# Optimization experiments

Measured on AMD Instinct MI355X. Metric: run time of the kernel, lower is better.

Reference implementation:

```python
import jax, jax.numpy as jnp
import numpy as np

N, E = 50000, 640000
DIN, DH, DOUT = 128, 256, 128


def _glorot(k, i, o):
    return jax.random.normal(k, (i, o), jnp.float32) / np.sqrt(i)


def setup_inputs() -> dict:
    key = jax.random.key(0)
    ks = jax.random.split(key, 12)
    return {
        "x": jax.random.normal(ks[0], (N, DIN), jnp.float32),
        "edge_index": jax.random.randint(ks[1], (2, E), 0, N, dtype=jnp.int32),
        # SAGEConv 1: in -> hidden (lin_l on aggregated w/ bias, lin_r on root)
        "W1l": _glorot(ks[2], DIN, DH), "b1l": jnp.zeros((DH,), jnp.float32), "W1r": _glorot(ks[3], DIN, DH),
        "g1": jnp.ones((DH,), jnp.float32), "be1": jnp.zeros((DH,), jnp.float32),
        # skip projection (in != hidden)
        "Wsk": _glorot(ks[4], DIN, DH), "bsk": jnp.zeros((DH,), jnp.float32),
        # SAGEConv 2: hidden -> hidden
        "W2l": _glorot(ks[5], DH, DH), "b2l": jnp.zeros((DH,), jnp.float32), "W2r": _glorot(ks[6], DH, DH),
        "g2": jnp.ones((DH,), jnp.float32), "be2": jnp.zeros((DH,), jnp.float32),
        # SAGEConv 3: hidden -> out
        "W3l": _glorot(ks[7], DH, DOUT), "b3l": jnp.zeros((DOUT,), jnp.float32), "W3r": _glorot(ks[8], DH, DOUT),
    }


def _sage_conv(x, src, dst, Wl, bl, Wr, n):
    # mean aggregation of source features into destination nodes
    msg = x[src]                                                 # [E, d]
    agg = jax.ops.segment_sum(msg, dst, num_segments=n)          # [N, d]
    cnt = jax.ops.segment_sum(jnp.ones((src.shape[0],), x.dtype), dst, num_segments=n)
    agg = agg / jnp.maximum(cnt, 1.0)[:, None]
    return agg @ Wl + bl + x @ Wr


def _layernorm(x, g, b):
    mu = jnp.mean(x, axis=-1, keepdims=True)
    var = jnp.mean((x - mu) ** 2, axis=-1, keepdims=True)
    return (x - mu) * jax.lax.rsqrt(var + 1e-5) * g + b


def reference(x, edge_index, W1l, b1l, W1r, g1, be1, Wsk, bsk,
              W2l, b2l, W2r, g2, be2, W3l, b3l, W3r):
    src, dst = edge_index[0], edge_index[1]
    n = x.shape[0]
    # layer 0: conv -> LN -> relu -> (dropout p=0, eval) -> skip via projection
    h = _sage_conv(x, src, dst, W1l, b1l, W1r, n)
    h = jax.nn.relu(_layernorm(h, g1, be1))
    h = h + (x @ Wsk + bsk)
    # layer 1: conv -> LN -> relu -> residual add (shapes match)
    h2 = _sage_conv(h, src, dst, W2l, b2l, W2r, n)
    h2 = jax.nn.relu(_layernorm(h2, g2, be2)) + h
    # final conv (no norm/act)
    return _sage_conv(h2, src, dst, W3l, b3l, W3r, n)
```

## Files before the change

### kernel.cpp

```cpp
#include <hip/hip_runtime.h>


typedef float floatx4 __attribute__((ext_vector_type(4)));
typedef short bf16x8 __attribute__((ext_vector_type(8)));

__device__ inline unsigned short f2bf(float f) {
    unsigned u = __float_as_uint(f);
    unsigned r = (u + 0x7fffu + ((u >> 16) & 1u)) >> 16;
    return (unsigned short)r;
}
__device__ inline float bf2f_lo(unsigned v) { return __uint_as_float(v << 16); }
__device__ inline float bf2f_hi(unsigned v) { return __uint_as_float(v & 0xffff0000u); }

__device__ inline void gl_lds16(const void* g, void* l) {
    __builtin_amdgcn_global_load_lds((const __attribute__((address_space(1))) unsigned int*)g,
                                     (__attribute__((address_space(3))) unsigned int*)l,
                                     16, 0, 0);
}

__global__ void hist_kernel(const int* __restrict__ dst, int* __restrict__ cnt, int E) {
    int i = blockIdx.x * blockDim.x + threadIdx.x;
    if (i < E) atomicAdd(&cnt[dst[i]], 1);
}

#define SCAN_CHUNK 2048

__global__ __launch_bounds__(256) void scan_blocksums(const int* __restrict__ cnt,
                                                      int* __restrict__ bsum, int N) {
    __shared__ int sh[256];
    int t = threadIdx.x;
    int base = blockIdx.x * SCAN_CHUNK + t * 8;
    int s = 0;
#pragma unroll
    for (int i = 0; i < 8; i++) {
        int idx = base + i;
        if (idx < N) s += cnt[idx];
    }
    sh[t] = s;
    __syncthreads();
    for (int off = 1; off < 256; off <<= 1) {
        int v = (t >= off) ? sh[t - off] : 0;
        __syncthreads();
        sh[t] += v;
        __syncthreads();
    }
    if (t == 255) bsum[blockIdx.x] = sh[255];
}

__global__ __launch_bounds__(256) void scan_bsums(const int* __restrict__ bsum,
                                                  int* __restrict__ boff, int NB,
                                                  int* __restrict__ rowptr, int N, int E) {
    __shared__ int sh[256];
    int t = threadIdx.x;
    int v = (t < NB) ? bsum[t] : 0;
    sh[t] = v;
    __syncthreads();
    for (int off = 1; off < 256; off <<= 1) {
        int u = (t >= off) ? sh[t - off] : 0;
        __syncthreads();
        sh[t] += u;
        __syncthreads();
    }
    if (t < NB) boff[t] = sh[t] - v;
    if (t == 0) rowptr[N] = E;
}

__global__ __launch_bounds__(256) void scan_final(const int* __restrict__ cnt,
                                                  const int* __restrict__ boff,
                                                  int* __restrict__ rowptr,
                                                  int* __restrict__ cursor,
                                                  float* __restrict__ invdeg, int N) {
    __shared__ int sh[256];
    int t = threadIdx.x;
    int base = blockIdx.x * SCAN_CHUNK + t * 8;
    int c[8];
    int s = 0;
#pragma unroll
    for (int i = 0; i < 8; i++) {
        int idx = base + i;
        c[i] = (idx < N) ? cnt[idx] : 0;
        s += c[i];
    }
    sh[t] = s;
    __syncthreads();
    for (int off = 1; off < 256; off <<= 1) {
        int v = (t >= off) ? sh[t - off] : 0;
        __syncthreads();
        sh[t] += v;
        __syncthreads();
    }
    int run = boff[blockIdx.x] + sh[t] - s;
#pragma unroll
    for (int i = 0; i < 8; i++) {
        int idx = base + i;
        if (idx < N) {
            rowptr[idx] = run;
            cursor[idx] = run;
            invdeg[idx] = 1.0f / (float)(c[i] > 1 ? c[i] : 1);
            run += c[i];
        }
    }
}

__global__ void scatter_kernel(const int* __restrict__ src, const int* __restrict__ dst,
                               int* __restrict__ cursor, int* __restrict__ col, int E) {
    int i = blockIdx.x * blockDim.x + threadIdx.x;
    if (i < E) {
        int p = atomicAdd(&cursor[dst[i]], 1);
        col[p] = src[i];
    }
}

__global__ void prep_weights(const float* __restrict__ W1l, const float* __restrict__ W1r,
                             const float* __restrict__ Wsk, const float* __restrict__ W2l,
                             const float* __restrict__ W2r, const float* __restrict__ W3l,
                             const float* __restrict__ W3r, const float* __restrict__ b1l,
                             const float* __restrict__ bsk,
                             unsigned short* __restrict__ WtC, unsigned short* __restrict__ Wt2,
                             unsigned short* __restrict__ Wt3, float* __restrict__ biasC) {
    int i = blockIdx.x * blockDim.x + threadIdx.x;
    if (i < 32768) {
        int k = i >> 8, n = i & 255;
        WtC[n * 256 + k] = f2bf(W1l[i]);
    } else if (i < 65536) {
        int j = i - 32768, k = j >> 8, n = j & 255;
        WtC[n * 256 + 128 + k] = f2bf(W1r[j]);
    } else if (i < 98304) {
        int j = i - 65536, k = j >> 8, n = j & 255;
        WtC[(256 + n) * 256 + 128 + k] = f2bf(Wsk[j]);
    } else if (i < 131072) {
        int j = i - 98304, k = j >> 8, n = j & 255;
        WtC[(256 + n) * 256 + k] = 0;
    } else if (i < 196608) {
        int j = i - 131072, k = j >> 8, n = j & 255;
        Wt2[n * 512 + k] = f2bf(W2l[j]);
    } else if (i < 262144) {
        int j = i - 196608, k = j >> 8, n = j & 255;
        Wt2[n * 512 + 256 + k] = f2bf(W2r[j]);
    } else if (i < 294912) {
        int j = i - 262144, k = j >> 7, n = j & 127;
        Wt3[n * 256 + k] = f2bf(W3l[j]);
    } else if (i < 327680) {
        int j = i - 294912, k = j >> 7, n = j & 127;
        Wt3[(128 + n) * 256 + k] = f2bf(W3r[j]);
    } else if (i < 328192) {
        int j = i - 327680;
        biasC[j] = (j < 256) ? b1l[j] : bsk[j - 256];
    }
}

__global__ void cvt_x_kernel(const float* __restrict__ x, unsigned short* __restrict__ A1cat, int total) {
    int i = blockIdx.x * blockDim.x + threadIdx.x;
    if (i >= total) return;
    int r = i >> 7, c = i & 127;
    A1cat[(size_t)r * 256 + 128 + c] = f2bf(x[i]);
}

__global__ __launch_bounds__(256) void agg_bf16_v2(const int* __restrict__ rowptr,
                                                   const int* __restrict__ col,
                                                   const float* __restrict__ invdeg,
                                                   const unsigned short* __restrict__ X, int xstride,
                                                   unsigned short* __restrict__ out, int ostride, int N) {
    int wid = (blockIdx.x * blockDim.x + threadIdx.x) >> 6;
    int lane = threadIdx.x & 63;
    if (wid >= N) return;
    int half = lane >> 5;
    int sub = lane & 31;
    int off = blockIdx.y * 128 + sub * 4;
    const unsigned short* Xo = X + off;
    int s = rowptr[wid], e = rowptr[wid + 1];
    float a0 = 0.f, a1 = 0.f, a2 = 0.f, a3 = 0.f;
    int j = s + half;
    for (; j + 6 < e; j += 8) {
        int c0 = col[j], c1 = col[j + 2], c2 = col[j + 4], c3 = col[j + 6];
        uint2 v0 = *(const uint2*)(Xo + (size_t)c0 * xstride);
        uint2 v1 = *(const uint2*)(Xo + (size_t)c1 * xstride);
        uint2 v2 = *(const uint2*)(Xo + (size_t)c2 * xstride);
        uint2 v3 = *(const uint2*)(Xo + (size_t)c3 * xstride);
        a0 += (bf2f_lo(v0.x) + bf2f_lo(v1.x)) + (bf2f_lo(v2.x) + bf2f_lo(v3.x));
        a1 += (bf2f_hi(v0.x) + bf2f_hi(v1.x)) + (bf2f_hi(v2.x) + bf2f_hi(v3.x));
        a2 += (bf2f_lo(v0.y) + bf2f_lo(v1.y)) + (bf2f_lo(v2.y) + bf2f_lo(v3.y));
        a3 += (bf2f_hi(v0.y) + bf2f_hi(v1.y)) + (bf2f_hi(v2.y) + bf2f_hi(v3.y));
    }
    for (; j < e; j += 2) {
        int c = col[j];
        uint2 v = *(const uint2*)(Xo + (size_t)c * xstride);
        a0 += bf2f_lo(v.x); a1 += bf2f_hi(v.x);
        a2 += bf2f_lo(v.y); a3 += bf2f_hi(v.y);
    }
    a0 += __shfl_xor(a0, 32, 64);
    a1 += __shfl_xor(a1, 32, 64);
    a2 += __shfl_xor(a2, 32, 64);
    a3 += __shfl_xor(a3, 32, 64);
    if (half == 0) {
        float inv = invdeg[wid];
        ushort4 o;
        o.x = f2bf(a0 * inv); o.y = f2bf(a1 * inv);
        o.z = f2bf(a2 * inv); o.w = f2bf(a3 * inv);
        *(ushort4*)(out + (size_t)wid * ostride + off) = o;
    }
}

__global__ __launch_bounds__(256) void agg_final_v2(const int* __restrict__ rowptr,
                                                    const int* __restrict__ col,
                                                    const float* __restrict__ invdeg,
                                                    const unsigned short* __restrict__ T,
                                                    const float* __restrict__ R,
                                                    float* __restrict__ out, int N) {
    int wid = (blockIdx.x * blockDim.x + threadIdx.x) >> 6;
    int lane = threadIdx.x & 63;
    if (wid >= N) return;
    int half = lane >> 5;
    int sub = lane & 31;
    const unsigned short* To = T + sub * 4;
    int s = rowptr[wid], e = rowptr[wid + 1];
    float a0 = 0.f, a1 = 0.f, a2 = 0.f, a3 = 0.f;
    int j = s + half;
    for (; j + 6 < e; j += 8) {
        int c0 = col[j], c1 = col[j + 2], c2 = col[j + 4], c3 = col[j + 6];
        uint2 v0 = *(const uint2*)(To + (size_t)c0 * 128);
        uint2 v1 = *(const uint2*)(To + (size_t)c1 * 128);
        uint2 v2 = *(const uint2*)(To + (size_t)c2 * 128);
        uint2 v3 = *(const uint2*)(To + (size_t)c3 * 128);
        a0 += (bf2f_lo(v0.x) + bf2f_lo(v1.x)) + (bf2f_lo(v2.x) + bf2f_lo(v3.x));
        a1 += (bf2f_hi(v0.x) + bf2f_hi(v1.x)) + (bf2f_hi(v2.x) + bf2f_hi(v3.x));
        a2 += (bf2f_lo(v0.y) + bf2f_lo(v1.y)) + (bf2f_lo(v2.y) + bf2f_lo(v3.y));
        a3 += (bf2f_hi(v0.y) + bf2f_hi(v1.y)) + (bf2f_hi(v2.y) + bf2f_hi(v3.y));
    }
    for (; j < e; j += 2) {
        int c = col[j];
        uint2 v = *(const uint2*)(To + (size_t)c * 128);
        a0 += bf2f_lo(v.x); a1 += bf2f_hi(v.x);
        a2 += bf2f_lo(v.y); a3 += bf2f_hi(v.y);
    }
    a0 += __shfl_xor(a0, 32, 64);
    a1 += __shfl_xor(a1, 32, 64);
    a2 += __shfl_xor(a2, 32, 64);
    a3 += __shfl_xor(a3, 32, 64);
    if (half == 0) {
        float inv = invdeg[wid];
        float4 r = *(const float4*)(R + (size_t)wid * 128 + sub * 4);
        float4 o;
        o.x = a0 * inv + r.x;
        o.y = a1 * inv + r.y;
        o.z = a2 * inv + r.z;
        o.w = a3 * inv + r.w;
        *(float4*)(out + (size_t)wid * 128 + sub * 4) = o;
    }
}

__device__ inline void store_out(float* p, float v) { *p = v; }
__device__ inline void store_out(unsigned short* p, float v) { *p = f2bf(v); }

template <typename OT>
__global__ __launch_bounds__(256) void gemm_mfma(const unsigned short* __restrict__ A, int lda, int K,
                                                 const unsigned short* __restrict__ B, int ldb,
                                                 const float* __restrict__ bias,
                                                 OT* __restrict__ C, int ldc, int M) {
    __shared__ unsigned short sA[128 * 64];
    __shared__ unsigned short sB[128 * 64];
    int t = threadIdx.x;
    int bm = blockIdx.x * 128;
    int bn = blockIdx.y * 128;
    int lane = t & 63;
    int w = t >> 6;
    int wm = (w >> 1) * 64, wn = (w & 1) * 64;

    floatx4 acc[4][4];
#pragma unroll
    for (int i = 0; i < 4; i++)
#pragma unroll
        for (int j = 0; j < 4; j++) acc[i][j] = (floatx4){0.f, 0.f, 0.f, 0.f};

    const int rA0 = t >> 3;
    const int kc8 = (t & 7) * 8;

    for (int k0 = 0; k0 < K; k0 += 64) {
#pragma unroll
        for (int i = 0; i < 4; i++) {
            int row = bm + rA0 + i * 32;
            if (row > M - 1) row = M - 1;
            gl_lds16(A + (size_t)row * lda + k0 + kc8, (void*)&sA[(size_t)(i * 256 + t) * 8]);
            gl_lds16(B + (size_t)(bn + rA0 + i * 32) * ldb + k0 + kc8,
                     (void*)&sB[(size_t)(i * 256 + t) * 8]);
        }
        __syncthreads();
#pragma unroll
        for (int ks = 0; ks < 2; ks++) {
            bf16x8 af[4], bfr[4];
#pragma unroll
            for (int mi = 0; mi < 4; mi++)
                af[mi] = *(const bf16x8*)&sA[(wm + mi * 16 + (lane & 15)) * 64 + ks * 32 + (lane >> 4) * 8];
#pragma unroll
            for (int ni = 0; ni < 4; ni++)
                bfr[ni] = *(const bf16x8*)&sB[(wn + ni * 16 + (lane & 15)) * 64 + ks * 32 + (lane >> 4) * 8];
#pragma unroll
            for (int mi = 0; mi < 4; mi++)
#pragma unroll
                for (int ni = 0; ni < 4; ni++)
                    acc[mi][ni] = __builtin_amdgcn_mfma_f32_16x16x32_bf16(af[mi], bfr[ni], acc[mi][ni], 0, 0, 0);
        }
        __syncthreads();
    }

    int col0 = bn + wn + (lane & 15);
    int rbase = bm + wm + (lane >> 4) * 4;
#pragma unroll
    for (int ni = 0; ni < 4; ni++) {
        int col = col0 + ni * 16;
        float bv = bias ? bias[col] : 0.f;
#pragma unroll
        for (int mi = 0; mi < 4; mi++) {
#pragma unroll
            for (int r = 0; r < 4; r++) {
                int row = rbase + mi * 16 + r;
                if (row < M) store_out(C + (size_t)row * ldc + col, acc[mi][ni][r] + bv);
            }
        }
    }
}

__global__ __launch_bounds__(256) void gemm_mfma_l3(const unsigned short* __restrict__ A, int lda, int K,
                                                    const unsigned short* __restrict__ B, int ldb,
                                                    const float* __restrict__ bias,
                                                    unsigned short* __restrict__ T,
                                                    float* __restrict__ R, int M) {
    __shared__ unsigned short sA[128 * 64];
    __shared__ unsigned short sB[128 * 64];
    int t = threadIdx.x;
    int bm = blockIdx.x * 128;
    int bn = blockIdx.y * 128;
    int lane = t & 63;
    int w = t >> 6;
    int wm = (w >> 1) * 64, wn = (w & 1) * 64;

    floatx4 acc[4][4];
#pragma unroll
    for (int i = 0; i < 4; i++)
#pragma unroll
        for (int j = 0; j < 4; j++) acc[i][j] = (floatx4){0.f, 0.f, 0.f, 0.f};

    const int rA0 = t >> 3;
    const int kc8 = (t & 7) * 8;

    for (int k0 = 0; k0 < K; k0 += 64) {
#pragma unroll
        for (int i = 0; i < 4; i++) {
            int row = bm + rA0 + i * 32;
            if (row > M - 1) row = M - 1;
            gl_lds16(A + (size_t)row * lda + k0 + kc8, (void*)&sA[(size_t)(i * 256 + t) * 8]);
            gl_lds16(B + (size_t)(bn + rA0 + i * 32) * ldb + k0 + kc8,
                     (void*)&sB[(size_t)(i * 256 + t) * 8]);
        }
        __syncthreads();
#pragma unroll
        for (int ks = 0; ks < 2; ks++) {
            bf16x8 af[4], bfr[4];
#pragma unroll
            for (int mi = 0; mi < 4; mi++)
                af[mi] = *(const bf16x8*)&sA[(wm + mi * 16 + (lane & 15)) * 64 + ks * 32 + (lane >> 4) * 8];
#pragma unroll
            for (int ni = 0; ni < 4; ni++)
                bfr[ni] = *(const bf16x8*)&sB[(wn + ni * 16 + (lane & 15)) * 64 + ks * 32 + (lane >> 4) * 8];
#pragma unroll
            for (int mi = 0; mi < 4; mi++)
#pragma unroll
                for (int ni = 0; ni < 4; ni++)
                    acc[mi][ni] = __builtin_amdgcn_mfma_f32_16x16x32_bf16(af[mi], bfr[ni], acc[mi][ni], 0, 0, 0);
        }
        __syncthreads();
    }

    int col0 = bn + wn + (lane & 15);
    int rbase = bm + wm + (lane >> 4) * 4;
#pragma unroll
    for (int ni = 0; ni < 4; ni++) {
        int col = col0 + ni * 16;
        if (col < 128) {
#pragma unroll
            for (int mi = 0; mi < 4; mi++)
#pragma unroll
                for (int r = 0; r < 4; r++) {
                    int row = rbase + mi * 16 + r;
                    if (row < M) T[(size_t)row * 128 + col] = f2bf(acc[mi][ni][r]);
                }
        } else {
            float bv = bias[col - 128];
#pragma unroll
            for (int mi = 0; mi < 4; mi++)
#pragma unroll
                for (int r = 0; r < 4; r++) {
                    int row = rbase + mi * 16 + r;
                    if (row < M) R[(size_t)row * 128 + col - 128] = acc[mi][ni][r] + bv;
                }
        }
    }
}

__global__ __launch_bounds__(256) void ln_fuse2(const unsigned short* __restrict__ u, int ustride,
                                                const unsigned short* __restrict__ a, int astride,
                                                const float* __restrict__ g, const float* __restrict__ b,
                                                unsigned short* __restrict__ out, int ostride, int N) {
    int row = (blockIdx.x * blockDim.x + threadIdx.x) >> 6;
    int lane = threadIdx.x & 63;
    if (row >= N) return;
    uint2 uv = *(const uint2*)(u + (size_t)row * ustride + lane * 4);
    float v0 = bf2f_lo(uv.x), v1 = bf2f_hi(uv.x), v2 = bf2f_lo(uv.y), v3 = bf2f_hi(uv.y);
    float s = (v0 + v1) + (v2 + v3);
    float sq = (v0 * v0 + v1 * v1) + (v2 * v2 + v3 * v3);
    for (int off = 1; off < 64; off <<= 1) {
        s += __shfl_xor(s, off, 64);
        sq += __shfl_xor(sq, off, 64);
    }
    float mu = s * (1.f / 256.f);
    float var = sq * (1.f / 256.f) - mu * mu;
    float rs = rsqrtf(var + 1e-5f);
    float4 gv = *(const float4*)(g + lane * 4);
    float4 bv = *(const float4*)(b + lane * 4);
    uint2 av = *(const uint2*)(a + (size_t)row * astride + lane * 4);
    float a0 = bf2f_lo(av.x), a1 = bf2f_hi(av.x), a2 = bf2f_lo(av.y), a3 = bf2f_hi(av.y);
    ushort4 o;
    o.x = f2bf(fmaxf((v0 - mu) * rs * gv.x + bv.x, 0.f) + a0);
    o.y = f2bf(fmaxf((v1 - mu) * rs * gv.y + bv.y, 0.f) + a1);
    o.z = f2bf(fmaxf((v2 - mu) * rs * gv.z + bv.z, 0.f) + a2);
    o.w = f2bf(fmaxf((v3 - mu) * rs * gv.w + bv.w, 0.f) + a3);
    *(ushort4*)(out + (size_t)row * ostride + lane * 4) = o;
}

extern "C" void kernel_launch(void* const* d_in, const int* in_sizes, int n_in,
                              void* d_out, int out_size, void* d_ws, size_t ws_size,
                              hipStream_t stream) {
    const float* x   = (const float*)d_in[0];
    const int*   ei  = (const int*)d_in[1];
    const float* W1l = (const float*)d_in[2];
    const float* b1l = (const float*)d_in[3];
    const float* W1r = (const float*)d_in[4];
    const float* g1  = (const float*)d_in[5];
    const float* be1 = (const float*)d_in[6];
    const float* Wsk = (const float*)d_in[7];
    const float* bsk = (const float*)d_in[8];
    const float* W2l = (const float*)d_in[9];
    const float* b2l = (const float*)d_in[10];
    const float* W2r = (const float*)d_in[11];
    const float* g2  = (const float*)d_in[12];
    const float* be2 = (const float*)d_in[13];
    const float* W3l = (const float*)d_in[14];
    const float* b3l = (const float*)d_in[15];
    const float* W3r = (const float*)d_in[16];

    const int N = in_sizes[0] / 128;
    const int E = in_sizes[1] / 2;
    const int* src = ei;
    const int* dst = ei + E;

    char* p = (char*)d_ws;
    auto alloc = [&](size_t bytes) {
        void* r = (void*)p;
        p += (bytes + 255) & ~(size_t)255;
        return r;
    };
    int*   cnt    = (int*)alloc(sizeof(int) * N);
    int*   rowptr = (int*)alloc(sizeof(int) * (N + 1));
    int*   cursor = (int*)alloc(sizeof(int) * N);
    float* invdeg = (float*)alloc(sizeof(float) * N);
    int*   col    = (int*)alloc(sizeof(int) * E);
    int*   bsum   = (int*)alloc(sizeof(int) * 256);
    int*   boff   = (int*)alloc(sizeof(int) * 256);
    unsigned short* A1cat = (unsigned short*)alloc(sizeof(short) * (size_t)N * 256);
    unsigned short* A2cat = (unsigned short*)alloc(sizeof(short) * (size_t)N * 512);
    unsigned short* U1    = (unsigned short*)alloc(sizeof(short) * (size_t)N * 512);
    float* r3 = (float*)alloc(sizeof(float) * (size_t)N * 128);
    unsigned short* WtC = (unsigned short*)alloc(sizeof(short) * 512 * 256);
    unsigned short* Wt2 = (unsigned short*)alloc(sizeof(short) * 256 * 512);
    unsigned short* Wt3 = (unsigned short*)alloc(sizeof(short) * 256 * 256);
    float* biasC = (float*)alloc(sizeof(float) * 512);
    unsigned short* t3 = A1cat;
    unsigned short* u2 = U1;

    hipMemsetAsync(cnt, 0, sizeof(int) * N, stream);
    hist_kernel<<<(E + 255) / 256, 256, 0, stream>>>(dst, cnt, E);
    int NB = (N + SCAN_CHUNK - 1) / SCAN_CHUNK;
    scan_blocksums<<<NB, 256, 0, stream>>>(cnt, bsum, N);
    scan_bsums<<<1, 256, 0, stream>>>(bsum, boff, NB, rowptr, N, E);
    scan_final<<<NB, 256, 0, stream>>>(cnt, boff, rowptr, cursor, invdeg, N);
    scatter_kernel<<<(E + 255) / 256, 256, 0, stream>>>(src, dst, cursor, col, E);

    prep_weights<<<(328192 + 255) / 256, 256, 0, stream>>>(W1l, W1r, Wsk, W2l, W2r, W3l, W3r,
                                                           b1l, bsk, WtC, Wt2, Wt3, biasC);
    cvt_x_kernel<<<((N * 128) + 255) / 256, 256, 0, stream>>>(x, A1cat, N * 128);

    int aggBlocks = (N + 3) / 4;
    int mBlocks = (N + 127) / 128;

    agg_bf16_v2<<<dim3(aggBlocks, 1), 256, 0, stream>>>(rowptr, col, invdeg, A1cat + 128, 256, A1cat, 256, N);
    gemm_mfma<unsigned short><<<dim3(mBlocks, 4), 256, 0, stream>>>(A1cat, 256, 256, WtC, 256, biasC, U1, 512, N);
    ln_fuse2<<<aggBlocks, 256, 0, stream>>>(U1, 512, U1 + 256, 512, g1, be1, A2cat + 256, 512, N);

    agg_bf16_v2<<<dim3(aggBlocks, 2), 256, 0, stream>>>(rowptr, col, invdeg, A2cat + 256, 512, A2cat, 512, N);
    gemm_mfma<unsigned short><<<dim3(mBlocks, 2), 256, 0, stream>>>(A2cat, 512, 512, Wt2, 512, b2l, u2, 256, N);
    ln_fuse2<<<aggBlocks, 256, 0, stream>>>(u2, 256, A2cat + 256, 512, g2, be2, A2cat, 512, N);

    gemm_mfma_l3<<<dim3(mBlocks, 2), 256, 0, stream>>>(A2cat, 512, 256, Wt3, 256, b3l, t3, r3, N);
    agg_final_v2<<<aggBlocks, 256, 0, stream>>>(rowptr, col, invdeg, t3, r3, (float*)d_out, N);
}
```

Baseline: 467.6 us.

## Replace LDS-tiled GEMMs with register-resident A-row GEMM reading weights directly

Replaces the 128x128 LDS-staged MFMA GEMM kernels with a single templated kernel. Each wave keeps a 16-row slice of A, covering the full K, in registers and streams weight fragments straight from global memory (L2-resident) across all N column groups. A is now read only once instead of once per column block, and the LDS staging and barriers are gone. In exchange there is more global traffic for B per wave, higher register pressure (up to 16 bf16x8 fragments for A), and uncoalesced 16-byte B loads.

```diff
diff --git a/kernel.cpp b/kernel.cpp
--- a/kernel.cpp
+++ b/kernel.cpp
@@ -11,12 +11,6 @@
 }
 __device__ inline float bf2f_lo(unsigned v) { return __uint_as_float(v << 16); }
 __device__ inline float bf2f_hi(unsigned v) { return __uint_as_float(v & 0xffff0000u); }
-
-__device__ inline void gl_lds16(const void* g, void* l) {
-    __builtin_amdgcn_global_load_lds((const __attribute__((address_space(1))) unsigned int*)g,
-                                     (__attribute__((address_space(3))) unsigned int*)l,
-                                     16, 0, 0);
-}
 
 __global__ void hist_kernel(const int* __restrict__ dst, int* __restrict__ cnt, int E) {
     int i = blockIdx.x * blockDim.x + threadIdx.x;
@@ -249,150 +243,65 @@
     }
 }
 
-__device__ inline void store_out(float* p, float v) { *p = v; }
-__device__ inline void store_out(unsigned short* p, float v) { *p = f2bf(v); }
-
-template <typename OT>
-__global__ __launch_bounds__(256) void gemm_mfma(const unsigned short* __restrict__ A, int lda, int K,
-                                                 const unsigned short* __restrict__ B, int ldb,
-                                                 const float* __restrict__ bias,
-                                                 OT* __restrict__ C, int ldc, int M) {
-    __shared__ unsigned short sA[128 * 64];
-    __shared__ unsigned short sB[128 * 64];
+template <int KSTEPS, int NGROUPS, int SPLIT>
+__global__ __launch_bounds__(256) void gemm_rs(const unsigned short* __restrict__ A, int lda,
+                                               const unsigned short* __restrict__ B, int ldb,
+                                               const float* __restrict__ bias,
+                                               unsigned short* __restrict__ C0, int ldc0,
+                                               float* __restrict__ C1, int M) {
     int t = threadIdx.x;
-    int bm = blockIdx.x * 128;
-    int bn = blockIdx.y * 128;
     int lane = t & 63;
     int w = t >> 6;
-    int wm = (w >> 1) * 64, wn = (w & 1) * 64;
-
-    floatx4 acc[4][4];
-#pragma unroll
-    for (int i = 0; i < 4; i++)
-#pragma unroll
-        for (int j = 0; j < 4; j++) acc[i][j] = (floatx4){0.f, 0.f, 0.f, 0.f};
-
-    const int rA0 = t >> 3;
-    const int kc8 = (t & 7) * 8;
-
-    for (int k0 = 0; k0 < K; k0 += 64) {
-#pragma unroll
-        for (int i = 0; i < 4; i++) {
-            int row = bm + rA0 + i * 32;
-            if (row > M - 1) row = M - 1;
-            gl_lds16(A + (size_t)row * lda + k0 + kc8, (void*)&sA[(size_t)(i * 256 + t) * 8]);
-            gl_lds16(B + (size_t)(bn + rA0 + i * 32) * ldb + k0 + kc8,
-                     (void*)&sB[(size_t)(i * 256 + t) * 8]);
-        }
-        __syncthreads();
-#pragma unroll
-        for (int ks = 0; ks < 2; ks++) {
-            bf16x8 af[4], bfr[4];
-#pragma unroll
-            for (int mi = 0; mi < 4; mi++)
-                af[mi] = *(const bf16x8*)&sA[(wm + mi * 16 + (lane & 15)) * 64 + ks * 32 + (lane >> 4) * 8];
-#pragma unroll
-            for (int ni = 0; ni < 4; ni++)
-                bfr[ni] = *(const bf16x8*)&sB[(wn + ni * 16 + (lane & 15)) * 64 + ks * 32 + (lane >> 4) * 8];
-#pragma unroll
-            for (int mi = 0; mi < 4; mi++)
-#pragma unroll
-                for (int ni = 0; ni < 4; ni++)
-                    acc[mi][ni] = __builtin_amdgcn_mfma_f32_16x16x32_bf16(af[mi], bfr[ni], acc[mi][ni], 0, 0, 0);
-        }
-        __syncthreads();
-    }
-
-    int col0 = bn + wn + (lane & 15);
-    int rbase = bm + wm + (lane >> 4) * 4;
-#pragma unroll
-    for (int ni = 0; ni < 4; ni++) {
-        int col = col0 + ni * 16;
-        float bv = bias ? bias[col] : 0.f;
-#pragma unroll
-        for (int mi = 0; mi < 4; mi++) {
-#pragma unroll
-            for (int r = 0; r < 4; r++) {
-                int row = rbase + mi * 16 + r;
-                if (row < M) store_out(C + (size_t)row * ldc + col, acc[mi][ni][r] + bv);
+    int row0 = blockIdx.x * 64 + w * 16;
+    int m16 = lane & 15;
+    int kq = lane >> 4;
+    int arow = row0 + m16;
+    if (arow > M - 1) arow = M - 1;
+
+    const unsigned short* Ap = A + (size_t)arow * lda + kq * 8;
+    bf16x8 a[KSTEPS];
+#pragma unroll
+    for (int ks = 0; ks < KSTEPS; ks++) a[ks] = *(const bf16x8*)(Ap + ks * 32);
+
+    int crow = kq * 4;
+#pragma unroll
+    for (int g = 0; g < NGROUPS; g++) {
+        int n0 = g * 128;
+        floatx4 acc[8];
+#pragma unroll
+        for (int nt = 0; nt < 8; nt++) acc[nt] = (floatx4){0.f, 0.f, 0.f, 0.f};
+#pragma unroll
+        for (int ks = 0; ks < KSTEPS; ks++) {
+#pragma unroll
+            for (int nt = 0; nt < 8; nt++) {
+                bf16x8 b = *(const bf16x8*)(B + (size_t)(n0 + nt * 16 + m16) * ldb + ks * 32 + kq * 8);
+                acc[nt] = __builtin_amdgcn_mfma_f32_16x16x32_bf16(a[ks], b, acc[nt], 0, 0, 0);
             }
         }
-    }
-}
-
-__global__ __launch_bounds__(256) void gemm_mfma_l3(const unsigned short* __restrict__ A, int lda, int K,
-                                                    const unsigned short* __restrict__ B, int ldb,
-                                                    const float* __restrict__ bias,
-                                                    unsigned short* __restrict__ T,
-                                                    float* __restrict__ R, int M) {
-    __shared__ unsigned short sA[128 * 64];
-    __shared__ unsigned short sB[128 * 64];
-    int t = threadIdx.x;
-    int bm = blockIdx.x * 128;
-    int bn = blockIdx.y * 128;
-    int lane = t & 63;
-    int w = t >> 6;
-    int wm = (w >> 1) * 64, wn = (w & 1) * 64;
-
-    floatx4 acc[4][4];
-#pragma unroll
-    for (int i = 0; i < 4; i++)
-#pragma unroll
-        for (int j = 0; j < 4; j++) acc[i][j] = (floatx4){0.f, 0.f, 0.f, 0.f};
-
-    const int rA0 = t >> 3;
-    const int kc8 = (t & 7) * 8;
-
-    for (int k0 = 0; k0 < K; k0 += 64) {
-#pragma unroll
-        for (int i = 0; i < 4; i++) {
-            int row = bm + rA0 + i * 32;
-            if (row > M - 1) row = M - 1;
-            gl_lds16(A + (size_t)row * lda + k0 + kc8, (void*)&sA[(size_t)(i * 256 + t) * 8]);
-            gl_lds16(B + (size_t)(bn + rA0 + i * 32) * ldb + k0 + kc8,
-                     (void*)&sB[(size_t)(i * 256 + t) * 8]);
-        }
-        __syncthreads();
-#pragma unroll
-        for (int ks = 0; ks < 2; ks++) {
-            bf16x8 af[4], bfr[4];
-#pragma unroll
-            for (int mi = 0; mi < 4; mi++)
-                af[mi] = *(const bf16x8*)&sA[(wm + mi * 16 + (lane & 15)) * 64 + ks * 32 + (lane >> 4) * 8];
-#pragma unroll
-            for (int ni = 0; ni < 4; ni++)
-                bfr[ni] = *(const bf16x8*)&sB[(wn + ni * 16 + (lane & 15)) * 64 + ks * 32 + (lane >> 4) * 8];
-#pragma unroll
-            for (int mi = 0; mi < 4; mi++)
-#pragma unroll
-                for (int ni = 0; ni < 4; ni++)
-                    acc[mi][ni] = __builtin_amdgcn_mfma_f32_16x16x32_bf16(af[mi], bfr[ni], acc[mi][ni], 0, 0, 0);
-        }
-        __syncthreads();
-    }
-
-    int col0 = bn + wn + (lane & 15);
-    int rbase = bm + wm + (lane >> 4) * 4;
-#pragma unroll
-    for (int ni = 0; ni < 4; ni++) {
-        int col = col0 + ni * 16;
-        if (col < 128) {
-#pragma unroll
-            for (int mi = 0; mi < 4; mi++)
+        if (SPLIT == 0 || g == 0) {
+            int ldc = (SPLIT == 0) ? ldc0 : 128;
+            int nc0 = (SPLIT == 0) ? n0 : 0;
+#pragma unroll
+            for (int nt = 0; nt < 8; nt++) {
+                float bv = (SPLIT == 0) ? bias[n0 + nt * 16 + m16] : 0.f;
 #pragma unroll
                 for (int r = 0; r < 4; r++) {
-                    int row = rbase + mi * 16 + r;
-                    if (row < M) T[(size_t)row * 128 + col] = f2bf(acc[mi][ni][r]);
+                    int grow = row0 + crow + r;
+                    if (grow < M)
+                        C0[(size_t)grow * ldc + nc0 + nt * 16 + m16] = f2bf(acc[nt][r] + bv);
                 }
+            }
         } else {
-            float bv = bias[col - 128];
-#pragma unroll
-            for (int mi = 0; mi < 4; mi++)
+#pragma unroll
+            for (int nt = 0; nt < 8; nt++) {
+                float bv = bias[nt * 16 + m16];
 #pragma unroll
                 for (int r = 0; r < 4; r++) {
-                    int row = rbase + mi * 16 + r;
-                    if (row < M) R[(size_t)row * 128 + col - 128] = acc[mi][ni][r] + bv;
+                    int grow = row0 + crow + r;
+                    if (grow < M)
+                        C1[(size_t)grow * 128 + nt * 16 + m16] = acc[nt][r] + bv;
                 }
+            }
         }
     }
 }
@@ -490,16 +399,16 @@
     cvt_x_kernel<<<((N * 128) + 255) / 256, 256, 0, stream>>>(x, A1cat, N * 128);
 
     int aggBlocks = (N + 3) / 4;
-    int mBlocks = (N + 127) / 128;
+    int gBlocks = (N + 63) / 64;
 
     agg_bf16_v2<<<dim3(aggBlocks, 1), 256, 0, stream>>>(rowptr, col, invdeg, A1cat + 128, 256, A1cat, 256, N);
-    gemm_mfma<unsigned short><<<dim3(mBlocks, 4), 256, 0, stream>>>(A1cat, 256, 256, WtC, 256, biasC, U1, 512, N);
+    gemm_rs<8, 4, 0><<<gBlocks, 256, 0, stream>>>(A1cat, 256, WtC, 256, biasC, U1, 512, nullptr, N);
     ln_fuse2<<<aggBlocks, 256, 0, stream>>>(U1, 512, U1 + 256, 512, g1, be1, A2cat + 256, 512, N);
 
     agg_bf16_v2<<<dim3(aggBlocks, 2), 256, 0, stream>>>(rowptr, col, invdeg, A2cat + 256, 512, A2cat, 512, N);
-    gemm_mfma<unsigned short><<<dim3(mBlocks, 2), 256, 0, stream>>>(A2cat, 512, 512, Wt2, 512, b2l, u2, 256, N);
+    gemm_rs<16, 2, 0><<<gBlocks, 256, 0, stream>>>(A2cat, 512, Wt2, 512, b2l, u2, 256, nullptr, N);
     ln_fuse2<<<aggBlocks, 256, 0, stream>>>(u2, 256, A2cat + 256, 512, g2, be2, A2cat, 512, N);
 
-    gemm_mfma_l3<<<dim3(mBlocks, 2), 256, 0, stream>>>(A2cat, 512, 256, Wt3, 256, b3l, t3, r3, N);
+    gemm_rs<8, 2, 1><<<gBlocks, 256, 0, stream>>>(A2cat, 512, Wt3, 256, b3l, t3, 128, r3, N);
     agg_final_v2<<<aggBlocks, 256, 0, stream>>>(rowptr, col, invdeg, t3, r3, (float*)d_out, N);
 }
```

Result: slower. 702.6 us (+50.3%).
